# Kernel optimization log

Measured on AMD Instinct MI355X. Metric: run time of the kernel, lower is better.

## Reference

```python
import jax, jax.numpy as jnp
import numpy as np

# dims: batch B, frames F_, spatial tokens N, heads H, head dim D, model dim DIM
B, F_, N, H, D, DIM = 1, 16, 1024, 8, 64, 512


def setup_inputs() -> dict:
    key = jax.random.key(0)
    k1, k2, k3, k4 = jax.random.split(key, 4)
    x = jax.random.normal(k1, (B, F_ * N, DIM), dtype=jnp.float32)
    W_qkv = jax.random.normal(k2, (DIM, 3 * H * D), dtype=jnp.float32) * 0.02
    W_out = jax.random.normal(k3, (H * D, DIM), dtype=jnp.float32) * 0.02
    mask = jax.random.randint(k4, (1, 1, N), 0, 2, dtype=jnp.int32)
    return {"x": x, "W_qkv": W_qkv, "W_out": W_out, "mask": mask, "diag": 1}


def reference(x, W_qkv, W_out, mask, diag):
    scale = D ** -0.5
    qkv = x @ W_qkv                      # [B, F*N, 3*H*D]
    q, k, v = jnp.split(qkv, 3, axis=-1)

    def split_heads(t):                  # 'b n (h d) -> (b h) n d'
        return t.reshape(B, F_ * N, H, D).transpose(0, 2, 1, 3).reshape(B * H, F_ * N, D)

    q, k, v = map(split_heads, (q, k, v))
    q = q * scale

    def axial(t):                        # '(b h) (f n) d -> (b h f) n d'
        return t.reshape(B * H * F_, N, D)

    q, k, v = map(axial, (q, k, v))

    sim = jnp.einsum('bid,bjd->bij', q, k)        # [(B*H*F), N, N]
    neg = -jnp.finfo(sim.dtype).max
    if diag:
        sim = jnp.where(jnp.eye(N, dtype=bool)[None], neg, sim)
    sim = jnp.where(mask == 0, neg, sim)           # padding mask broadcast
    attn = jax.nn.softmax(sim, axis=-1)
    out = jnp.einsum('bij,bjd->bid', attn, v)      # [(B*H*F), N, D]

    # '(b h f) n d -> (b h) (f n) d' then '(b h) n d -> b n (h d)'
    out = out.reshape(B, H, F_ * N, D).transpose(0, 2, 1, 3).reshape(B, F_ * N, H * D)
    return out @ W_out
```

## Files before the change

kernel.cpp:

```cpp
#include <hip/hip_runtime.h>
#include <stdint.h>

typedef __bf16 bf16;
typedef __bf16 bf16x8 __attribute__((ext_vector_type(8)));
typedef float f32x4 __attribute__((ext_vector_type(4)));

__device__ __forceinline__ void gload_lds16(const void* g, void* l) {
    __builtin_amdgcn_global_load_lds((const __attribute__((address_space(1))) void*)g,
                                     (__attribute__((address_space(3))) void*)l, 16, 0, 0);
}

__device__ __forceinline__ float fast_exp2(float x) { return __builtin_amdgcn_exp2f(x); }

__global__ __launch_bounds__(256) void k_prep(const float* __restrict__ x, bf16* __restrict__ xb,
                                              const float* __restrict__ Wqkv, bf16* __restrict__ WqT,
                                              const float* __restrict__ Wout, bf16* __restrict__ WoT,
                                              const int* __restrict__ mask, int* __restrict__ idxU,
                                              int* __restrict__ cpos, int* __restrict__ meta) {
    __shared__ float t[32][33];
    __shared__ int lsum[256];
    int b = blockIdx.x, tid = threadIdx.x;
    if (b < 4096) {
        int i = b * 256 + tid;
        const f32x4* p = (const f32x4*)(x + (size_t)i * 8);
        f32x4 a = p[0], c = p[1];
        bf16x8 o;
        o[0] = (bf16)a[0]; o[1] = (bf16)a[1]; o[2] = (bf16)a[2]; o[3] = (bf16)a[3];
        o[4] = (bf16)c[0]; o[5] = (bf16)c[1]; o[6] = (bf16)c[2]; o[7] = (bf16)c[3];
        *(bf16x8*)(xb + (size_t)i * 8) = o;
    } else if (b < 4096 + 768 + 256) {
        const float* W; bf16* WT; int C, bb;
        if (b < 4096 + 768) { W = Wqkv; WT = WqT; C = 1536; bb = b - 4096;    }
        else                { W = Wout; WT = WoT; C = 512;  bb = b - 4864;    }
        int nblk = C / 32;
        int n0 = (bb % nblk) * 32, k0 = (bb / nblk) * 32;
        int tx = tid & 31, ty = tid >> 5;
        for (int i = 0; i < 32; i += 8) t[ty + i][tx] = W[(size_t)(k0 + ty + i) * C + n0 + tx];
        __syncthreads();
        for (int i = 0; i < 32; i += 8) WT[(size_t)(n0 + ty + i) * 512 + k0 + tx] = (bf16)t[tx][ty + i];
    } else {
        int m[4], s = 0;
#pragma unroll
        for (int e = 0; e < 4; e++) { m[e] = mask[4 * tid + e]; s += m[e]; }
        lsum[tid] = s;
        __syncthreads();
        for (int off = 1; off < 256; off <<= 1) {
            int v = (tid >= off) ? lsum[tid - off] : 0;
            __syncthreads();
            lsum[tid] += v;
            __syncthreads();
        }
        int run = lsum[tid] - s;
#pragma unroll
        for (int e = 0; e < 4; e++) {
            if (m[e]) { idxU[run] = 4 * tid + e; cpos[4 * tid + e] = run; run++; }
            else cpos[4 * tid + e] = -1;
        }
        int nU = lsum[255];
        for (int i = nU + tid; i < 1024; i += 256) idxU[i] = 0;
        if (tid == 255) { meta[0] = nU; meta[1] = (nU + 63) >> 6; }
    }
}

__global__ __launch_bounds__(256) void k_qkv(const bf16* __restrict__ Xb, const bf16* __restrict__ WT,
                                             bf16* __restrict__ Qb, bf16* __restrict__ Kb, bf16* __restrict__ Vb) {
    __shared__ char As[16384], Bs[16384];
    int tid = threadIdx.x, l = tid & 63, w = tid >> 6;
    int wy = w >> 1, wx = w & 1;
    int id = blockIdx.x;
    int wg = (id & 7) * 192 + (id >> 3);
    int bm = (wg / 12) * 128, bn = (wg % 12) * 128;
    int lr = l & 15, kg = l >> 4;
    int p = l & 7, rsub = l >> 3;
    int csrc = p ^ rsub;
    f32x4 acc[4][4] = {};

    for (int k0 = 0; k0 < 512; k0 += 64) {
        __syncthreads();
#pragma unroll
        for (int i = 0; i < 4; i++) {
            int rt = w * 32 + i * 8 + rsub;
            gload_lds16((const char*)Xb + ((size_t)(bm + rt) * 512 + k0) * 2 + csrc * 16,
                        As + w * 4096 + i * 1024 + l * 16);
            gload_lds16((const char*)WT + ((size_t)(bn + rt) * 512 + k0) * 2 + csrc * 16,
                        Bs + w * 4096 + i * 1024 + l * 16);
        }
        __syncthreads();
#pragma unroll
        for (int kk = 0; kk < 2; kk++) {
            bf16x8 af[4], bfr[4];
            int sb = (kk * 4 + kg);
#pragma unroll
            for (int mt = 0; mt < 4; mt++) {
                int r = wy * 64 + mt * 16 + lr;
                af[mt] = *(const bf16x8*)(As + r * 128 + ((sb ^ (lr & 7)) << 4));
            }
#pragma unroll
            for (int nt = 0; nt < 4; nt++) {
                int r = wx * 64 + nt * 16 + lr;
                bfr[nt] = *(const bf16x8*)(Bs + r * 128 + ((sb ^ (lr & 7)) << 4));
            }
#pragma unroll
            for (int mt = 0; mt < 4; mt++)
#pragma unroll
                for (int nt = 0; nt < 4; nt++)
                    acc[mt][nt] = __builtin_amdgcn_mfma_f32_16x16x32_bf16(af[mt], bfr[nt], acc[mt][nt], 0, 0, 0);
        }
    }
#pragma unroll
    for (int mt = 0; mt < 4; mt++) {
#pragma unroll
        for (int nt = 0; nt < 4; nt++) {
            int c = bn + wx * 64 + nt * 16 + lr;
            int which = c >> 9, hd = c & 511, h = hd >> 6, d = hd & 63;
            float qs = (which == 0) ? 0.18033688f : 1.0f;
            bf16* base = (which == 0) ? Qb : (which == 1) ? Kb : Vb;
#pragma unroll
            for (int j = 0; j < 4; j++) {
                int m = bm + wy * 64 + mt * 16 + kg * 4 + j;
                int f = m >> 10, nn = m & 1023;
                base[((size_t)(h * 16 + f) * 1024 + nn) * 64 + d] = (bf16)(acc[mt][nt][j] * qs);
            }
        }
    }
}

__global__ __launch_bounds__(256) void k_vtg(const bf16* __restrict__ V, bf16* __restrict__ Vtc,
                                             const int* __restrict__ idxU, const int* __restrict__ meta) {
    __shared__ bf16 t[64][80];
    int bp = blockIdx.y, c0 = blockIdx.x * 64;
    int nU = meta[0], nUp = meta[1] << 6;
    if (c0 >= nUp) return;
    int tid = threadIdx.x;
    int nl = tid >> 2, dc = (tid & 3) * 16;
    int c = c0 + nl;
    bf16x8 a0 = {}, a1 = {};
    if (c < nU) {
        int row = idxU[c];
        const bf16* src = V + ((size_t)bp * 1024 + row) * 64 + dc;
        a0 = *(const bf16x8*)src;
        a1 = *(const bf16x8*)(src + 8);
    }
    *(bf16x8*)&t[nl][dc] = a0;
    *(bf16x8*)&t[nl][dc + 8] = a1;
    __syncthreads();
    int dl = tid >> 2, nc = (tid & 3) * 16;
    bf16x8 o0, o1;
#pragma unroll
    for (int i = 0; i < 8; i++) o0[i] = t[nc + i][dl];
#pragma unroll
    for (int i = 0; i < 8; i++) o1[i] = t[nc + 8 + i][dl];
    bf16* dst = Vtc + ((size_t)bp * 64 + dl) * 1024 + c0 + nc;
    *(bf16x8*)dst = o0;
    *(bf16x8*)(dst + 8) = o1;
}

__global__ __launch_bounds__(512) void k_attn(const bf16* __restrict__ Qb, const bf16* __restrict__ Kb,
                                              const bf16* __restrict__ Vtc, bf16* __restrict__ AO,
                                              const int* __restrict__ cpos, const int* __restrict__ idxU,
                                              const int* __restrict__ meta, const int* __restrict__ diagp) {
    __shared__ char Ks[8192], Vs[8192], Ps[16384];
    int tid = threadIdx.x, l = tid & 63, w = tid >> 6;
    int id = blockIdx.x;
    int wg = (id & 7) * 128 + (id >> 3);
    int qt = wg & 7, bp = wg >> 3;
    int lr = l & 15, kg = l >> 4;
    int diag = diagp[0];
    int nU = meta[0], nT = meta[1];

    int nq = qt * 128 + w * 16 + lr;
    const char* Qrow = (const char*)Qb + ((size_t)bp * 1024 + nq) * 128;
    bf16x8 qf0 = *(const bf16x8*)(Qrow + kg * 16);
    bf16x8 qf1 = *(const bf16x8*)(Qrow + 64 + kg * 16);

    int cq[4];
#pragma unroll
    for (int j = 0; j < 4; j++) {
        int qg = qt * 128 + w * 16 + kg * 4 + j;
        cq[j] = diag ? cpos[qg] : -1;
    }

    const char* Kbb = (const char*)Kb + (size_t)bp * 1024 * 128;
    const char* Vbase = (const char*)Vtc + (size_t)bp * 64 * 2048;

    int rs = tid >> 3;
    int cs = (tid & 7) ^ (rs & 7);

    f32x4 o[4] = {};
    f32x4 psum = {0.f, 0.f, 0.f, 0.f};

    for (int kt = 0; kt < nT; kt++) {
        __syncthreads();
        int krow = idxU[kt * 64 + rs];
        gload_lds16(Kbb + (size_t)krow * 128 + cs * 16, Ks + w * 1024);
        gload_lds16(Vbase + (size_t)rs * 2048 + kt * 128 + cs * 16, Vs + w * 1024);
        __syncthreads();

        f32x4 s[4] = {};
        __builtin_amdgcn_s_setprio(1);
#pragma unroll
        for (int nt = 0; nt < 4; nt++) {
            int r = nt * 16 + lr;
            bf16x8 kf0 = *(const bf16x8*)(Ks + r * 128 + ((kg ^ (r & 7)) << 4));
            bf16x8 kf1 = *(const bf16x8*)(Ks + r * 128 + (((4 + kg) ^ (r & 7)) << 4));
            s[nt] = __builtin_amdgcn_mfma_f32_16x16x32_bf16(qf0, kf0, s[nt], 0, 0, 0);
            s[nt] = __builtin_amdgcn_mfma_f32_16x16x32_bf16(qf1, kf1, s[nt], 0, 0, 0);
        }
        __builtin_amdgcn_s_setprio(0);

        float mf0 = (kt * 64 + lr < nU) ? 1.f : 0.f;
        float mf1 = (kt * 64 + 16 + lr < nU) ? 1.f : 0.f;
        float mf2 = (kt * 64 + 32 + lr < nU) ? 1.f : 0.f;
        float mf3 = (kt * 64 + 48 + lr < nU) ? 1.f : 0.f;
#pragma unroll
        for (int j = 0; j < 4; j++) {
            s[0][j] = fast_exp2(s[0][j]) * mf0;
            s[1][j] = fast_exp2(s[1][j]) * mf1;
            s[2][j] = fast_exp2(s[2][j]) * mf2;
            s[3][j] = fast_exp2(s[3][j]) * mf3;
        }
#pragma unroll
        for (int nt = 0; nt < 4; nt++) {
            int c = kt * 64 + nt * 16 + lr;
#pragma unroll
            for (int j = 0; j < 4; j++)
                if (c == cq[j]) s[nt][j] = 0.f;
        }
#pragma unroll
        for (int j = 0; j < 4; j++) psum[j] += (s[0][j] + s[1][j]) + (s[2][j] + s[3][j]);

#pragma unroll
        for (int nt = 0; nt < 4; nt++)
#pragma unroll
            for (int j = 0; j < 4; j++) {
                int rq = w * 16 + kg * 4 + j;
                int byte = (rq * 128 + (nt * 16 + lr) * 2) ^ ((rq & 7) << 4);
                *(bf16*)(Ps + byte) = (bf16)s[nt][j];
            }

        int rp = w * 16 + lr;
        bf16x8 pf0 = *(const bf16x8*)(Ps + rp * 128 + ((kg ^ (rp & 7)) << 4));
        bf16x8 pf1 = *(const bf16x8*)(Ps + rp * 128 + (((4 + kg) ^ (rp & 7)) << 4));
        __builtin_amdgcn_s_setprio(1);
#pragma unroll
        for (int dt = 0; dt < 4; dt++) {
            int rd = dt * 16 + lr;
            bf16x8 vf0 = *(const bf16x8*)(Vs + rd * 128 + ((kg ^ (rd & 7)) << 4));
            bf16x8 vf1 = *(const bf16x8*)(Vs + rd * 128 + (((4 + kg) ^ (rd & 7)) << 4));
            o[dt] = __builtin_amdgcn_mfma_f32_16x16x32_bf16(pf0, vf0, o[dt], 0, 0, 0);
            o[dt] = __builtin_amdgcn_mfma_f32_16x16x32_bf16(pf1, vf1, o[dt], 0, 0, 0);
        }
        __builtin_amdgcn_s_setprio(0);
    }

#pragma unroll
    for (int off = 1; off < 16; off <<= 1)
#pragma unroll
        for (int j = 0; j < 4; j++) psum[j] += __shfl_xor(psum[j], off, 64);
    float inv[4];
#pragma unroll
    for (int j = 0; j < 4; j++) inv[j] = 1.0f / psum[j];

    int f = bp & 15, h = bp >> 4;
#pragma unroll
    for (int dt = 0; dt < 4; dt++)
#pragma unroll
        for (int j = 0; j < 4; j++) {
            int n = qt * 128 + w * 16 + kg * 4 + j;
            size_t m = (size_t)f * 1024 + n;
            AO[m * 512 + h * 64 + dt * 16 + lr] = (bf16)(o[dt][j] * inv[j]);
        }
}

__global__ __launch_bounds__(256) void k_out(const bf16* __restrict__ Ab, const bf16* __restrict__ WT,
                                             float* __restrict__ out) {
    __shared__ char As[16384], Bs[16384];
    int tid = threadIdx.x, l = tid & 63, w = tid >> 6;
    int wy = w >> 1, wx = w & 1;
    int id = blockIdx.x;
    int wg = (id & 7) * 64 + (id >> 3);
    int bm = (wg / 4) * 128, bn = (wg % 4) * 128;
    int lr = l & 15, kg = l >> 4;
    int p = l & 7, rsub = l >> 3;
    int csrc = p ^ rsub;
    f32x4 acc[4][4] = {};

    for (int k0 = 0; k0 < 512; k0 += 64) {
        __syncthreads();
#pragma unroll
        for (int i = 0; i < 4; i++) {
            int rt = w * 32 + i * 8 + rsub;
            gload_lds16((const char*)Ab + ((size_t)(bm + rt) * 512 + k0) * 2 + csrc * 16,
                        As + w * 4096 + i * 1024 + l * 16);
            gload_lds16((const char*)WT + ((size_t)(bn + rt) * 512 + k0) * 2 + csrc * 16,
                        Bs + w * 4096 + i * 1024 + l * 16);
        }
        __syncthreads();
#pragma unroll
        for (int kk = 0; kk < 2; kk++) {
            bf16x8 af[4], bfr[4];
            int sb = (kk * 4 + kg);
#pragma unroll
            for (int mt = 0; mt < 4; mt++) {
                int r = wy * 64 + mt * 16 + lr;
                af[mt] = *(const bf16x8*)(As + r * 128 + ((sb ^ (lr & 7)) << 4));
            }
#pragma unroll
            for (int nt = 0; nt < 4; nt++) {
                int r = wx * 64 + nt * 16 + lr;
                bfr[nt] = *(const bf16x8*)(Bs + r * 128 + ((sb ^ (lr & 7)) << 4));
            }
#pragma unroll
            for (int mt = 0; mt < 4; mt++)
#pragma unroll
                for (int nt = 0; nt < 4; nt++)
                    acc[mt][nt] = __builtin_amdgcn_mfma_f32_16x16x32_bf16(af[mt], bfr[nt], acc[mt][nt], 0, 0, 0);
        }
    }
#pragma unroll
    for (int mt = 0; mt < 4; mt++)
#pragma unroll
        for (int nt = 0; nt < 4; nt++) {
            int c = bn + wx * 64 + nt * 16 + lr;
#pragma unroll
            for (int j = 0; j < 4; j++) {
                int m = bm + wy * 64 + mt * 16 + kg * 4 + j;
                out[(size_t)m * 512 + c] = acc[mt][nt][j];
            }
        }
}

extern "C" void kernel_launch(void* const* d_in, const int* in_sizes, int n_in,
                              void* d_out, int out_size, void* d_ws, size_t ws_size,
                              hipStream_t stream) {
    const float* x    = (const float*)d_in[0];
    const float* Wqkv = (const float*)d_in[1];
    const float* Wout = (const float*)d_in[2];
    const int*   mask = (const int*)d_in[3];
    const int*   diag = (const int*)d_in[4];
    float* out = (float*)d_out;
    char* ws = (char*)d_ws;

    bf16* Xb  = (bf16*)(ws);
    bf16* Vtc = (bf16*)(ws);
    bf16* WqT = (bf16*)(ws + ((size_t)16 << 20));
    bf16* WoT = (bf16*)(ws + ((size_t)18 << 20));
    int*  idxU = (int*)(ws + ((size_t)18 << 20) + (1 << 19));
    int*  cpos = (int*)(ws + ((size_t)18 << 20) + (1 << 19) + 4096);
    int*  meta = (int*)(ws + ((size_t)18 << 20) + (1 << 19) + 8192);
    bf16* Qb  = (bf16*)(ws + ((size_t)19 << 20));
    bf16* Kb  = (bf16*)(ws + ((size_t)35 << 20));
    bf16* Vb  = (bf16*)(ws + ((size_t)51 << 20));
    bf16* AO  = (bf16*)(ws + ((size_t)67 << 20));

    hipLaunchKernelGGL(k_prep, dim3(4096 + 768 + 256 + 1), dim3(256), 0, stream,
                       x, Xb, Wqkv, WqT, Wout, WoT, mask, idxU, cpos, meta);
    hipLaunchKernelGGL(k_qkv, dim3(1536), dim3(256), 0, stream, Xb, WqT, Qb, Kb, Vb);
    hipLaunchKernelGGL(k_vtg, dim3(16, 128), dim3(256), 0, stream, Vb, Vtc, idxU, meta);
    hipLaunchKernelGGL(k_attn, dim3(1024), dim3(512), 0, stream, Qb, Kb, Vtc, AO, cpos, idxU, meta, diag);
    hipLaunchKernelGGL(k_out, dim3(512), dim3(256), 0, stream, AO, WoT, out);
}
```

Measured before the change: 113.8 us.

## Gather unmasked key rows in QKV GEMM and skip masked K/V projection tiles

The QKV projection now computes K and V only for unmasked key positions. It gathers their X rows through idxU and returns early for tiles beyond the padded count of valid keys, writing compacted K and V buffers. The attention and V-transpose kernels then read the compacted buffers contiguously instead of indirecting through idxU. This cuts K/V GEMM work roughly in proportion to the mask density and removes gather loads from the attention inner loop. The cost is an indirect A-row address computation per tile and workgroups that exit early, which can leave the grid unevenly loaded.

```diff
diff --git a/kernel.cpp b/kernel.cpp
--- a/kernel.cpp
+++ b/kernel.cpp
@@ -30,8 +30,8 @@
         *(bf16x8*)(xb + (size_t)i * 8) = o;
     } else if (b < 4096 + 768 + 256) {
         const float* W; bf16* WT; int C, bb;
-        if (b < 4096 + 768) { W = Wqkv; WT = WqT; C = 1536; bb = b - 4096;    }
-        else                { W = Wout; WT = WoT; C = 512;  bb = b - 4864;    }
+        if (b < 4096 + 768) { W = Wqkv; WT = WqT; C = 1536; bb = b - 4096; }
+        else                { W = Wout; WT = WoT; C = 512;  bb = b - 4864; }
         int nblk = C / 32;
         int n0 = (bb % nblk) * 32, k0 = (bb / nblk) * 32;
         int tx = tid & 31, ty = tid >> 5;
@@ -62,25 +62,44 @@
     }
 }
 
-__global__ __launch_bounds__(256) void k_qkv(const bf16* __restrict__ Xb, const bf16* __restrict__ WT,
-                                             bf16* __restrict__ Qb, bf16* __restrict__ Kb, bf16* __restrict__ Vb) {
+__global__ __launch_bounds__(256) void k_qkv2(const bf16* __restrict__ Xb, const bf16* __restrict__ WT,
+                                              bf16* __restrict__ Qb, bf16* __restrict__ Kc,
+                                              bf16* __restrict__ Vc, const int* __restrict__ idxU,
+                                              const int* __restrict__ meta) {
     __shared__ char As[16384], Bs[16384];
     int tid = threadIdx.x, l = tid & 63, w = tid >> 6;
     int wy = w >> 1, wx = w & 1;
     int id = blockIdx.x;
     int wg = (id & 7) * 192 + (id >> 3);
-    int bm = (wg / 12) * 128, bn = (wg % 12) * 128;
     int lr = l & 15, kg = l >> 4;
     int p = l & 7, rsub = l >> 3;
     int csrc = p ^ rsub;
+
+    bool qmode = wg < 512;
+    int bm, bn;
+    if (qmode) { bm = (wg >> 2) * 128; bn = (wg & 3) * 128; }
+    else {
+        int wgk = wg - 512;
+        bm = (wgk >> 3) * 128; bn = 512 + (wgk & 7) * 128;
+        int nUp = meta[1] << 6;
+        if ((bm & 1023) >= nUp) return;
+    }
+
+    size_t srcA[4];
+#pragma unroll
+    for (int i = 0; i < 4; i++) {
+        int m = bm + w * 32 + i * 8 + rsub;
+        int row = qmode ? m : ((m & ~1023) + idxU[m & 1023]);
+        srcA[i] = (size_t)row * 512;
+    }
+
     f32x4 acc[4][4] = {};
-
     for (int k0 = 0; k0 < 512; k0 += 64) {
         __syncthreads();
 #pragma unroll
         for (int i = 0; i < 4; i++) {
             int rt = w * 32 + i * 8 + rsub;
-            gload_lds16((const char*)Xb + ((size_t)(bm + rt) * 512 + k0) * 2 + csrc * 16,
+            gload_lds16((const char*)Xb + (srcA[i] + k0) * 2 + csrc * 16,
                         As + w * 4096 + i * 1024 + l * 16);
             gload_lds16((const char*)WT + ((size_t)(bn + rt) * 512 + k0) * 2 + csrc * 16,
                         Bs + w * 4096 + i * 1024 + l * 16);
@@ -107,26 +126,39 @@
                     acc[mt][nt] = __builtin_amdgcn_mfma_f32_16x16x32_bf16(af[mt], bfr[nt], acc[mt][nt], 0, 0, 0);
         }
     }
-#pragma unroll
-    for (int mt = 0; mt < 4; mt++) {
-#pragma unroll
-        for (int nt = 0; nt < 4; nt++) {
-            int c = bn + wx * 64 + nt * 16 + lr;
-            int which = c >> 9, hd = c & 511, h = hd >> 6, d = hd & 63;
-            float qs = (which == 0) ? 0.18033688f : 1.0f;
-            bf16* base = (which == 0) ? Qb : (which == 1) ? Kb : Vb;
+
+    int cb = bn + wx * 64;
+    if (qmode) {
+        int h = cb >> 6;
+#pragma unroll
+        for (int mt = 0; mt < 4; mt++)
 #pragma unroll
             for (int j = 0; j < 4; j++) {
                 int m = bm + wy * 64 + mt * 16 + kg * 4 + j;
                 int f = m >> 10, nn = m & 1023;
-                base[((size_t)(h * 16 + f) * 1024 + nn) * 64 + d] = (bf16)(acc[mt][nt][j] * qs);
-            }
-        }
-    }
-}
-
-__global__ __launch_bounds__(256) void k_vtg(const bf16* __restrict__ V, bf16* __restrict__ Vtc,
-                                             const int* __restrict__ idxU, const int* __restrict__ meta) {
+#pragma unroll
+                for (int nt = 0; nt < 4; nt++)
+                    Qb[((size_t)(h * 16 + f) * 1024 + nn) * 64 + nt * 16 + lr] =
+                        (bf16)(acc[mt][nt][j] * 0.18033688f);
+            }
+    } else {
+        int which = cb >> 9, hd = cb & 511, h = hd >> 6;
+        bf16* base = (which == 1) ? Kc : Vc;
+#pragma unroll
+        for (int mt = 0; mt < 4; mt++)
+#pragma unroll
+            for (int j = 0; j < 4; j++) {
+                int m = bm + wy * 64 + mt * 16 + kg * 4 + j;
+                int f = m >> 10, cc = m & 1023;
+#pragma unroll
+                for (int nt = 0; nt < 4; nt++)
+                    base[((size_t)(h * 16 + f) * 1024 + cc) * 64 + nt * 16 + lr] = (bf16)acc[mt][nt][j];
+            }
+    }
+}
+
+__global__ __launch_bounds__(256) void k_vtg(const bf16* __restrict__ Vc, bf16* __restrict__ Vtc,
+                                             const int* __restrict__ meta) {
     __shared__ bf16 t[64][80];
     int bp = blockIdx.y, c0 = blockIdx.x * 64;
     int nU = meta[0], nUp = meta[1] << 6;
@@ -136,8 +168,7 @@
     int c = c0 + nl;
     bf16x8 a0 = {}, a1 = {};
     if (c < nU) {
-        int row = idxU[c];
-        const bf16* src = V + ((size_t)bp * 1024 + row) * 64 + dc;
+        const bf16* src = Vc + ((size_t)bp * 1024 + c) * 64 + dc;
         a0 = *(const bf16x8*)src;
         a1 = *(const bf16x8*)(src + 8);
     }
@@ -155,10 +186,10 @@
     *(bf16x8*)(dst + 8) = o1;
 }
 
-__global__ __launch_bounds__(512) void k_attn(const bf16* __restrict__ Qb, const bf16* __restrict__ Kb,
+__global__ __launch_bounds__(512) void k_attn(const bf16* __restrict__ Kq, const bf16* __restrict__ Kc,
                                               const bf16* __restrict__ Vtc, bf16* __restrict__ AO,
-                                              const int* __restrict__ cpos, const int* __restrict__ idxU,
-                                              const int* __restrict__ meta, const int* __restrict__ diagp) {
+                                              const int* __restrict__ cpos, const int* __restrict__ meta,
+                                              const int* __restrict__ diagp) {
     __shared__ char Ks[8192], Vs[8192], Ps[16384];
     int tid = threadIdx.x, l = tid & 63, w = tid >> 6;
     int id = blockIdx.x;
@@ -169,7 +200,7 @@
     int nU = meta[0], nT = meta[1];
 
     int nq = qt * 128 + w * 16 + lr;
-    const char* Qrow = (const char*)Qb + ((size_t)bp * 1024 + nq) * 128;
+    const char* Qrow = (const char*)Kq + ((size_t)bp * 1024 + nq) * 128;
     bf16x8 qf0 = *(const bf16x8*)(Qrow + kg * 16);
     bf16x8 qf1 = *(const bf16x8*)(Qrow + 64 + kg * 16);
 
@@ -180,7 +211,7 @@
         cq[j] = diag ? cpos[qg] : -1;
     }
 
-    const char* Kbb = (const char*)Kb + (size_t)bp * 1024 * 128;
+    const char* Kbase = (const char*)Kc + (size_t)bp * 1024 * 128;
     const char* Vbase = (const char*)Vtc + (size_t)bp * 64 * 2048;
 
     int rs = tid >> 3;
@@ -191,8 +222,7 @@
 
     for (int kt = 0; kt < nT; kt++) {
         __syncthreads();
-        int krow = idxU[kt * 64 + rs];
-        gload_lds16(Kbb + (size_t)krow * 128 + cs * 16, Ks + w * 1024);
+        gload_lds16(Kbase + (size_t)(kt * 64 + rs) * 128 + cs * 16, Ks + w * 1024);
         gload_lds16(Vbase + (size_t)rs * 2048 + kt * 128 + cs * 16, Vs + w * 1024);
         __syncthreads();
 
@@ -349,14 +379,14 @@
     int*  cpos = (int*)(ws + ((size_t)18 << 20) + (1 << 19) + 4096);
     int*  meta = (int*)(ws + ((size_t)18 << 20) + (1 << 19) + 8192);
     bf16* Qb  = (bf16*)(ws + ((size_t)19 << 20));
-    bf16* Kb  = (bf16*)(ws + ((size_t)35 << 20));
-    bf16* Vb  = (bf16*)(ws + ((size_t)51 << 20));
+    bf16* Kc  = (bf16*)(ws + ((size_t)35 << 20));
+    bf16* Vc  = (bf16*)(ws + ((size_t)51 << 20));
     bf16* AO  = (bf16*)(ws + ((size_t)67 << 20));
 
     hipLaunchKernelGGL(k_prep, dim3(4096 + 768 + 256 + 1), dim3(256), 0, stream,
                        x, Xb, Wqkv, WqT, Wout, WoT, mask, idxU, cpos, meta);
-    hipLaunchKernelGGL(k_qkv, dim3(1536), dim3(256), 0, stream, Xb, WqT, Qb, Kb, Vb);
-    hipLaunchKernelGGL(k_vtg, dim3(16, 128), dim3(256), 0, stream, Vb, Vtc, idxU, meta);
-    hipLaunchKernelGGL(k_attn, dim3(1024), dim3(512), 0, stream, Qb, Kb, Vtc, AO, cpos, idxU, meta, diag);
+    hipLaunchKernelGGL(k_qkv2, dim3(1536), dim3(256), 0, stream, Xb, WqT, Qb, Kc, Vc, idxU, meta);
+    hipLaunchKernelGGL(k_vtg, dim3(16, 128), dim3(256), 0, stream, Vc, Vtc, meta);
+    hipLaunchKernelGGL(k_attn, dim3(1024), dim3(512), 0, stream, Qb, Kc, Vtc, AO, cpos, meta, diag);
     hipLaunchKernelGGL(k_out, dim3(512), dim3(256), 0, stream, AO, WoT, out);
 }
```

After: 115.0 us. Within noise of the previous version (+1.1%).

## Double-buffer LDS tiles in QKV GEMM to overlap global loads with MFMA

Applied to the files above, without the earlier changes.

Rewrites the QKV projection GEMM main loop to use two LDS buffers with K-step 32 instead of a single buffer with K-step 64. The next tile's global-to-LDS loads are issued before computing the current tile, so memory latency can overlap with MFMA work, and the loop needs only one barrier per iteration. The LDS swizzle is changed to match the 64-byte row layout. The cost is twice as many loop iterations, each with less compute per barrier.

```diff
diff --git a/kernel.cpp b/kernel.cpp
--- a/kernel.cpp
+++ b/kernel.cpp
@@ -30,8 +30,8 @@
         *(bf16x8*)(xb + (size_t)i * 8) = o;
     } else if (b < 4096 + 768 + 256) {
         const float* W; bf16* WT; int C, bb;
-        if (b < 4096 + 768) { W = Wqkv; WT = WqT; C = 1536; bb = b - 4096;    }
-        else                { W = Wout; WT = WoT; C = 512;  bb = b - 4864;    }
+        if (b < 4096 + 768) { W = Wqkv; WT = WqT; C = 1536; bb = b - 4096; }
+        else                { W = Wout; WT = WoT; C = 512;  bb = b - 4864; }
         int nblk = C / 32;
         int n0 = (bb % nblk) * 32, k0 = (bb / nblk) * 32;
         int tx = tid & 31, ty = tid >> 5;
@@ -64,49 +64,56 @@
 
 __global__ __launch_bounds__(256) void k_qkv(const bf16* __restrict__ Xb, const bf16* __restrict__ WT,
                                              bf16* __restrict__ Qb, bf16* __restrict__ Kb, bf16* __restrict__ Vb) {
-    __shared__ char As[16384], Bs[16384];
+    __shared__ char As[2][8192], Bs[2][8192];
     int tid = threadIdx.x, l = tid & 63, w = tid >> 6;
     int wy = w >> 1, wx = w & 1;
     int id = blockIdx.x;
     int wg = (id & 7) * 192 + (id >> 3);
     int bm = (wg / 12) * 128, bn = (wg % 12) * 128;
     int lr = l & 15, kg = l >> 4;
-    int p = l & 7, rsub = l >> 3;
-    int csrc = p ^ rsub;
+
+    int subr = l >> 2, chk = l & 3;
+    int R0 = w * 32 + subr,     m0 = (R0 >> 1) & 3, c0 = chk ^ m0;
+    int R1 = w * 32 + 16 + subr, m1 = (R1 >> 1) & 3, c1 = chk ^ m1;
+
     f32x4 acc[4][4] = {};
 
-    for (int k0 = 0; k0 < 512; k0 += 64) {
-        __syncthreads();
-#pragma unroll
-        for (int i = 0; i < 4; i++) {
-            int rt = w * 32 + i * 8 + rsub;
-            gload_lds16((const char*)Xb + ((size_t)(bm + rt) * 512 + k0) * 2 + csrc * 16,
-                        As + w * 4096 + i * 1024 + l * 16);
-            gload_lds16((const char*)WT + ((size_t)(bn + rt) * 512 + k0) * 2 + csrc * 16,
-                        Bs + w * 4096 + i * 1024 + l * 16);
-        }
-        __syncthreads();
-#pragma unroll
-        for (int kk = 0; kk < 2; kk++) {
-            bf16x8 af[4], bfr[4];
-            int sb = (kk * 4 + kg);
-#pragma unroll
-            for (int mt = 0; mt < 4; mt++) {
-                int r = wy * 64 + mt * 16 + lr;
-                af[mt] = *(const bf16x8*)(As + r * 128 + ((sb ^ (lr & 7)) << 4));
-            }
-#pragma unroll
-            for (int nt = 0; nt < 4; nt++) {
-                int r = wx * 64 + nt * 16 + lr;
-                bfr[nt] = *(const bf16x8*)(Bs + r * 128 + ((sb ^ (lr & 7)) << 4));
-            }
-#pragma unroll
-            for (int mt = 0; mt < 4; mt++)
-#pragma unroll
-                for (int nt = 0; nt < 4; nt++)
-                    acc[mt][nt] = __builtin_amdgcn_mfma_f32_16x16x32_bf16(af[mt], bfr[nt], acc[mt][nt], 0, 0, 0);
-        }
-    }
+    gload_lds16((const char*)Xb + ((size_t)(bm + R0) * 512) * 2 + c0 * 16, As[0] + w * 2048 + l * 16);
+    gload_lds16((const char*)Xb + ((size_t)(bm + R1) * 512) * 2 + c1 * 16, As[0] + w * 2048 + 1024 + l * 16);
+    gload_lds16((const char*)WT + ((size_t)(bn + R0) * 512) * 2 + c0 * 16, Bs[0] + w * 2048 + l * 16);
+    gload_lds16((const char*)WT + ((size_t)(bn + R1) * 512) * 2 + c1 * 16, Bs[0] + w * 2048 + 1024 + l * 16);
+    __syncthreads();
+
+    for (int t = 0; t < 16; t++) {
+        int cur = t & 1;
+        if (t < 15) {
+            int k1 = (t + 1) * 32;
+            gload_lds16((const char*)Xb + ((size_t)(bm + R0) * 512 + k1) * 2 + c0 * 16, As[cur ^ 1] + w * 2048 + l * 16);
+            gload_lds16((const char*)Xb + ((size_t)(bm + R1) * 512 + k1) * 2 + c1 * 16, As[cur ^ 1] + w * 2048 + 1024 + l * 16);
+            gload_lds16((const char*)WT + ((size_t)(bn + R0) * 512 + k1) * 2 + c0 * 16, Bs[cur ^ 1] + w * 2048 + l * 16);
+            gload_lds16((const char*)WT + ((size_t)(bn + R1) * 512 + k1) * 2 + c1 * 16, Bs[cur ^ 1] + w * 2048 + 1024 + l * 16);
+        }
+
+        bf16x8 af[4], bfr[4];
+#pragma unroll
+        for (int mt = 0; mt < 4; mt++) {
+            int r = wy * 64 + mt * 16 + lr;
+            af[mt] = *(const bf16x8*)(As[cur] + r * 64 + ((kg ^ ((r >> 1) & 3)) << 4));
+        }
+#pragma unroll
+        for (int nt = 0; nt < 4; nt++) {
+            int r = wx * 64 + nt * 16 + lr;
+            bfr[nt] = *(const bf16x8*)(Bs[cur] + r * 64 + ((kg ^ ((r >> 1) & 3)) << 4));
+        }
+#pragma unroll
+        for (int mt = 0; mt < 4; mt++)
+#pragma unroll
+            for (int nt = 0; nt < 4; nt++)
+                acc[mt][nt] = __builtin_amdgcn_mfma_f32_16x16x32_bf16(af[mt], bfr[nt], acc[mt][nt], 0, 0, 0);
+
+        __syncthreads();
+    }
+
 #pragma unroll
     for (int mt = 0; mt < 4; mt++) {
 #pragma unroll
```

Measured after the change: 110.3 us. 3.0% less time.
